# Kernel optimization log

Hardware: AMD Instinct MI355X
Metric: run time of the kernel (lower is better)

The kernel has to match this reference:

```python
import jax, jax.numpy as jnp
import numpy as np

H, T, D = 16, 4096, 64
N_SEQ = 8  # packed sequences -> cu_seqlens has N_SEQ+1 entries


def setup_inputs() -> dict:
    key = jax.random.key(0)
    kq, kk, kv, kc = jax.random.split(key, 4)
    q = jax.random.normal(kq, (1, H, T, D), dtype=jnp.float32)
    k = jax.random.normal(kk, (1, H, T, D), dtype=jnp.float32)
    v = jax.random.normal(kv, (1, H, T, D), dtype=jnp.float32)
    # cu_seqlens: monotonically increasing offsets, starts at 0, ends at T
    interior = jnp.sort(jax.random.randint(kc, (N_SEQ - 1,), 1, T, dtype=jnp.int32))
    cu_seqlens = jnp.concatenate([
        jnp.zeros((1,), jnp.int32), interior, jnp.full((1,), T, jnp.int32)
    ])
    return {"q": q, "k": k, "v": v, "cu_seqlens": cu_seqlens}


def reference(q, k, v, cu_seqlens):
    # Faithful to flash_attn_varlen_func(..., causal=False) on packed sequences:
    # non-causal attention restricted block-diagonally to each segment.
    scale = 1.0 / jnp.sqrt(jnp.asarray(D, q.dtype))
    # segment id for every token position
    pos = jnp.arange(T)
    seg = jnp.searchsorted(cu_seqlens[1:], pos, side="right")  # [T]
    mask = seg[:, None] == seg[None, :]                         # [T, T] block-diagonal
    # scores: [1, H, T, T]
    scores = jnp.einsum("bhqd,bhkd->bhqk", q, k) * scale
    neg = jnp.asarray(jnp.finfo(scores.dtype).min, scores.dtype)
    scores = jnp.where(mask[None, None], scores, neg)
    attn = jax.nn.softmax(scores, axis=-1)
    out = jnp.einsum("bhqk,bhkd->bhqd", attn, v)  # [1, H, T, D]
    return out
```

## Files before the change

kernel.cpp:

```cpp
#include <hip/hip_runtime.h>

#define HH 16
#define TT 4096
#define DD 64

typedef __attribute__((ext_vector_type(2))) __fp16 half2r;
typedef __attribute__((ext_vector_type(4))) _Float16 half4;
typedef __attribute__((ext_vector_type(4))) float float4v;

__global__ __launch_bounds__(256, 4) void pa_fwd(
    const float* __restrict__ qg, const float* __restrict__ kg,
    const float* __restrict__ vg, const int* __restrict__ cu,
    float* __restrict__ outg)
{
    __shared__ __align__(16) _Float16 Kl[2][64 * 64];
    __shared__ __align__(16) _Float16 Vl[2][64 * 64];

    const int tid  = threadIdx.x;
    const int lane = tid & 63;
    const int wave = tid >> 6;
    const int lr   = lane & 15;
    const int lg   = lane >> 4;

    const int bswz = ((int)blockIdx.x & 7) * 128 + ((int)blockIdx.x >> 3);
    const int h    = bswz >> 6;
    const int qblk = (bswz & 63) << 6;
    const int q    = qblk + wave * 16 + lr;

    int s = 0;
    while (cu[s + 1] <= q) ++s;
    const int lo = cu[s], hi = cu[s + 1];

    int sb = 0;
    while (cu[sb + 1] <= qblk) ++sb;
    const int blo = cu[sb];
    while (cu[sb + 1] <= qblk + 63) ++sb;
    const int bhi = cu[sb + 1];

    const int wlo = __shfl(lo, 0);
    const int whi = __shfl(hi, 15);
    const int mlo = __shfl(lo, 15);
    const int mhi = __shfl(hi, 0);

    const float qscale = 0.125f * 1.44269504088896f;
    const float* qrow = qg + ((size_t)h * TT + q) * DD;
    half4 qf[4];
#pragma unroll
    for (int ds = 0; ds < 4; ++ds) {
        float4v t4 = *(const float4v*)(qrow + ds * 16 + lg * 4);
        half2r a = __builtin_amdgcn_cvt_pkrtz(t4[0] * qscale, t4[1] * qscale);
        half2r b = __builtin_amdgcn_cvt_pkrtz(t4[2] * qscale, t4[3] * qscale);
        qf[ds][0] = (_Float16)a[0]; qf[ds][1] = (_Float16)a[1];
        qf[ds][2] = (_Float16)b[0]; qf[ds][3] = (_Float16)b[1];
    }

    const float* kh_ = kg + (size_t)h * TT * DD;
    const float* vh_ = vg + (size_t)h * TT * DD;

    const int srow = tid >> 2;
    const int sch  = (tid & 3) << 4;
    const int vd   = tid & 63;

    unsigned kwr[4], vwr[4];
#pragma unroll
    for (int i = 0; i < 4; ++i) {
        const int ko8 = (tid & 3) * 4 + i;
        kwr[i] = (unsigned)(srow * 128 + 16 * ((ko8 >> 1) ^ (srow & 7)) +
                            8 * ((ko8 & 1) ^ ((srow >> 3) & 1)));
        const int vo8 = wave * 4 + i;
        vwr[i] = (unsigned)(vd * 128 + 16 * ((vo8 >> 1) ^ (vd & 7)) +
                            8 * ((vo8 & 1) ^ ((vd >> 3) & 1)));
    }
    unsigned rbase[4];
#pragma unroll
    for (int i = 0; i < 4; ++i)
        rbase[i] = (unsigned)(lr * 128 + 16 * (((2 * i + (lg >> 1))) ^ (lr & 7)) +
                              8 * ((lg & 1) ^ ((lr >> 3) & 1)));

    float4v kq[4];
    float vv[16];

#define ISSUE(KT)                                                              \
    {                                                                          \
        const float4v* kp = (const float4v*)(kh_ + (size_t)((KT) + srow) * DD + sch); \
        kq[0] = kp[0]; kq[1] = kp[1]; kq[2] = kp[2]; kq[3] = kp[3];            \
        const float* vp = vh_ + (size_t)((KT) + wave * 16) * DD + vd;          \
        _Pragma("unroll")                                                      \
        for (int c = 0; c < 16; ++c) vv[c] = vp[c * DD];                       \
    }

    const int t0k = blo & ~63;
    ISSUE(t0k);

    float4v acc[4];
#pragma unroll
    for (int dt = 0; dt < 4; ++dt) acc[dt] = (float4v){0.f, 0.f, 0.f, 0.f};
    float m_run = -1e30f, lsum = 0.f;

    int cur = 0;
    for (int kt = t0k; kt < bhi; kt += 64) {
        {
            char* Kb = (char*)Kl[cur];
            char* Vb = (char*)Vl[cur];
#pragma unroll
            for (int i = 0; i < 4; ++i) {
                half2r a = __builtin_amdgcn_cvt_pkrtz(kq[i][0], kq[i][1]);
                half2r b = __builtin_amdgcn_cvt_pkrtz(kq[i][2], kq[i][3]);
                half4 hk;
                hk[0] = (_Float16)a[0]; hk[1] = (_Float16)a[1];
                hk[2] = (_Float16)b[0]; hk[3] = (_Float16)b[1];
                *(half4*)(Kb + kwr[i]) = hk;
            }
#pragma unroll
            for (int i = 0; i < 4; ++i) {
                half2r a = __builtin_amdgcn_cvt_pkrtz(vv[4 * i], vv[4 * i + 1]);
                half2r b = __builtin_amdgcn_cvt_pkrtz(vv[4 * i + 2], vv[4 * i + 3]);
                half4 hv;
                hv[0] = (_Float16)a[0]; hv[1] = (_Float16)a[1];
                hv[2] = (_Float16)b[0]; hv[3] = (_Float16)b[1];
                *(half4*)(Vb + vwr[i]) = hv;
            }
        }
        __syncthreads();

        if (kt + 64 < bhi) ISSUE(kt + 64);

        if (!(kt + 64 <= wlo || kt >= whi)) {
            const char* Kb = (const char*)Kl[cur];
            const char* Vb = (const char*)Vl[cur];

            float st[4][4];
            const bool fullv = (kt >= mlo) && (kt + 64 <= mhi);
            __builtin_amdgcn_s_setprio(1);
#pragma unroll
            for (int t = 0; t < 4; ++t) {
                float4v sa = (float4v){0.f, 0.f, 0.f, 0.f};
#pragma unroll
                for (int ds = 0; ds < 4; ++ds) {
                    half4 kf = *(const half4*)(Kb + rbase[ds] + t * 2048);
                    sa = __builtin_amdgcn_mfma_f32_16x16x16f16(kf, qf[ds], sa, 0, 0, 0);
                }
                if (fullv) {
#pragma unroll
                    for (int j = 0; j < 4; ++j) st[t][j] = sa[j];
                } else {
#pragma unroll
                    for (int j = 0; j < 4; ++j) {
                        const int key = kt + t * 16 + lg * 4 + j;
                        st[t][j] = (key >= lo && key < hi) ? sa[j] : -1e30f;
                    }
                }
            }
            __builtin_amdgcn_s_setprio(0);

            float tx = -1e30f;
#pragma unroll
            for (int t = 0; t < 4; ++t)
#pragma unroll
                for (int j = 0; j < 4; ++j) tx = fmaxf(tx, st[t][j]);
            tx = fmaxf(tx, __shfl_xor(tx, 16));
            tx = fmaxf(tx, __shfl_xor(tx, 32));

            if (__any(tx > m_run + 11.54f)) {
                const float mn = fmaxf(m_run, tx);
                const float a  = exp2f(m_run - mn);
                lsum *= a;
#pragma unroll
                for (int dt = 0; dt < 4; ++dt)
#pragma unroll
                    for (int j = 0; j < 4; ++j) acc[dt][j] *= a;
                m_run = mn;
            }

            half4 pb[4];
            float ps = 0.f;
#pragma unroll
            for (int t = 0; t < 4; ++t) {
                float e0 = exp2f(st[t][0] - m_run);
                float e1 = exp2f(st[t][1] - m_run);
                float e2 = exp2f(st[t][2] - m_run);
                float e3 = exp2f(st[t][3] - m_run);
                ps += (e0 + e1) + (e2 + e3);
                half2r a = __builtin_amdgcn_cvt_pkrtz(e0, e1);
                half2r b = __builtin_amdgcn_cvt_pkrtz(e2, e3);
                pb[t][0] = (_Float16)a[0]; pb[t][1] = (_Float16)a[1];
                pb[t][2] = (_Float16)b[0]; pb[t][3] = (_Float16)b[1];
            }
            ps += __shfl_xor(ps, 16);
            ps += __shfl_xor(ps, 32);
            lsum += ps;

            __builtin_amdgcn_s_setprio(1);
#pragma unroll
            for (int t = 0; t < 4; ++t)
#pragma unroll
                for (int dt = 0; dt < 4; ++dt) {
                    half4 vf = *(const half4*)(Vb + rbase[t] + dt * 2048);
                    acc[dt] = __builtin_amdgcn_mfma_f32_16x16x16f16(vf, pb[t], acc[dt], 0, 0, 0);
                }
            __builtin_amdgcn_s_setprio(0);
        }
        cur ^= 1;
    }

    const float inv = 1.0f / lsum;
    float* orow = outg + ((size_t)h * TT + q) * DD;
#pragma unroll
    for (int dt = 0; dt < 4; ++dt) {
        float4v o;
#pragma unroll
        for (int j = 0; j < 4; ++j) o[j] = acc[dt][j] * inv;
        *(float4v*)(orow + dt * 16 + lg * 4) = o;
    }
#undef ISSUE
}

extern "C" void kernel_launch(void* const* d_in, const int* in_sizes, int n_in,
                              void* d_out, int out_size, void* d_ws, size_t ws_size,
                              hipStream_t stream) {
    const float* q  = (const float*)d_in[0];
    const float* k  = (const float*)d_in[1];
    const float* v  = (const float*)d_in[2];
    const int*   cu = (const int*)d_in[3];
    float* out = (float*)d_out;

    dim3 grid(HH * (TT / 64));
    dim3 block(256);
    hipLaunchKernelGGL(pa_fwd, grid, block, 0, stream, q, k, v, cu, out);
}
```

Baseline: 90.51 us.

## Use 16x16x32 MFMA for QK^T and vectorize K/V LDS staging

Replaces the four 16x16x16 f16 MFMAs per score tile with two 16x16x32 MFMAs, loading K fragments as 8-wide halves from LDS and Q as half8. It also restructures the global-to-LDS staging: K/V are written as 16-byte half8 stores with a new XOR swizzle, V is loaded as float2 pairs, and pointers are advanced incrementally instead of being recomputed. The goal is to cut MFMA issue count, LDS instruction count and address arithmetic. The price is a new swizzle layout that must stay consistent between the write and read paths.

```diff
diff --git a/kernel.cpp b/kernel.cpp
--- a/kernel.cpp
+++ b/kernel.cpp
@@ -6,6 +6,8 @@
 
 typedef __attribute__((ext_vector_type(2))) __fp16 half2r;
 typedef __attribute__((ext_vector_type(4))) _Float16 half4;
+typedef __attribute__((ext_vector_type(8))) _Float16 half8;
+typedef __attribute__((ext_vector_type(2))) float float2v;
 typedef __attribute__((ext_vector_type(4))) float float4v;
 
 __global__ __launch_bounds__(256, 4) void pa_fwd(
@@ -44,53 +46,59 @@
 
     const float qscale = 0.125f * 1.44269504088896f;
     const float* qrow = qg + ((size_t)h * TT + q) * DD;
-    half4 qf[4];
-#pragma unroll
-    for (int ds = 0; ds < 4; ++ds) {
-        float4v t4 = *(const float4v*)(qrow + ds * 16 + lg * 4);
-        half2r a = __builtin_amdgcn_cvt_pkrtz(t4[0] * qscale, t4[1] * qscale);
-        half2r b = __builtin_amdgcn_cvt_pkrtz(t4[2] * qscale, t4[3] * qscale);
-        qf[ds][0] = (_Float16)a[0]; qf[ds][1] = (_Float16)a[1];
-        qf[ds][2] = (_Float16)b[0]; qf[ds][3] = (_Float16)b[1];
+    half8 qf8[2];
+#pragma unroll
+    for (int ds = 0; ds < 2; ++ds) {
+        const float* qp = qrow + ds * 32 + lg * 8;
+        float4v a = *(const float4v*)qp;
+        float4v b = *(const float4v*)(qp + 4);
+        half2r p0 = __builtin_amdgcn_cvt_pkrtz(a[0] * qscale, a[1] * qscale);
+        half2r p1 = __builtin_amdgcn_cvt_pkrtz(a[2] * qscale, a[3] * qscale);
+        half2r p2 = __builtin_amdgcn_cvt_pkrtz(b[0] * qscale, b[1] * qscale);
+        half2r p3 = __builtin_amdgcn_cvt_pkrtz(b[2] * qscale, b[3] * qscale);
+        qf8[ds][0] = (_Float16)p0[0]; qf8[ds][1] = (_Float16)p0[1];
+        qf8[ds][2] = (_Float16)p1[0]; qf8[ds][3] = (_Float16)p1[1];
+        qf8[ds][4] = (_Float16)p2[0]; qf8[ds][5] = (_Float16)p2[1];
+        qf8[ds][6] = (_Float16)p3[0]; qf8[ds][7] = (_Float16)p3[1];
     }
 
     const float* kh_ = kg + (size_t)h * TT * DD;
     const float* vh_ = vg + (size_t)h * TT * DD;
 
     const int srow = tid >> 2;
-    const int sch  = (tid & 3) << 4;
-    const int vd   = tid & 63;
-
-    unsigned kwr[4], vwr[4];
-#pragma unroll
-    for (int i = 0; i < 4; ++i) {
-        const int ko8 = (tid & 3) * 4 + i;
-        kwr[i] = (unsigned)(srow * 128 + 16 * ((ko8 >> 1) ^ (srow & 7)) +
-                            8 * ((ko8 & 1) ^ ((srow >> 3) & 1)));
-        const int vo8 = wave * 4 + i;
-        vwr[i] = (unsigned)(vd * 128 + 16 * ((vo8 >> 1) ^ (vd & 7)) +
-                            8 * ((vo8 & 1) ^ ((vd >> 3) & 1)));
-    }
-    unsigned rbase[4];
-#pragma unroll
-    for (int i = 0; i < 4; ++i)
-        rbase[i] = (unsigned)(lr * 128 + 16 * (((2 * i + (lg >> 1))) ^ (lr & 7)) +
-                              8 * ((lg & 1) ^ ((lr >> 3) & 1)));
+    const int sc   = tid & 3;
+    const unsigned kwrA = (unsigned)(srow * 128 + (((2 * sc)     ^ (srow & 7)) << 4));
+    const unsigned kwrB = (unsigned)(srow * 128 + (((2 * sc + 1) ^ (srow & 7)) << 4));
+    const int vd2 = tid & 31;
+    const int vko = tid >> 5;
+    const int vr0 = 2 * vd2, vr1 = 2 * vd2 + 1;
+    const unsigned vwrA = (unsigned)(vr0 * 128 + ((vko ^ (vr0 & 7)) << 4));
+    const unsigned vwrB = (unsigned)(vr1 * 128 + ((vko ^ (vr1 & 7)) << 4));
+
+    const unsigned kb0 = (unsigned)(lr * 128 + (((lg)     ^ (lr & 7)) << 4));
+    const unsigned kb1 = (unsigned)(lr * 128 + (((4 + lg) ^ (lr & 7)) << 4));
+    unsigned vrb[4];
+#pragma unroll
+    for (int t = 0; t < 4; ++t)
+        vrb[t] = (unsigned)(lr * 128 + (((2 * t + (lg >> 1)) ^ (lr & 7)) << 4) +
+                            ((lg & 1) << 3));
 
     float4v kq[4];
-    float vv[16];
-
-#define ISSUE(KT)                                                              \
+    float2v vv2[8];
+    const int t0k = blo & ~63;
+    const float4v* kp = (const float4v*)(kh_ + (size_t)(t0k + srow) * DD + sc * 16);
+    const float*   vp = vh_ + (size_t)(t0k + vko * 8) * DD + vd2 * 2;
+
+#define ISSUE()                                                                \
     {                                                                          \
-        const float4v* kp = (const float4v*)(kh_ + (size_t)((KT) + srow) * DD + sch); \
         kq[0] = kp[0]; kq[1] = kp[1]; kq[2] = kp[2]; kq[3] = kp[3];            \
-        const float* vp = vh_ + (size_t)((KT) + wave * 16) * DD + vd;          \
+        kp += (64 * DD) / 4;                                                   \
         _Pragma("unroll")                                                      \
-        for (int c = 0; c < 16; ++c) vv[c] = vp[c * DD];                       \
-    }
-
-    const int t0k = blo & ~63;
-    ISSUE(t0k);
+        for (int c = 0; c < 8; ++c) vv2[c] = *(const float2v*)(vp + c * DD);   \
+        vp += 64 * DD;                                                         \
+    }
+
+    ISSUE();
 
     float4v acc[4];
 #pragma unroll
@@ -102,28 +110,33 @@
         {
             char* Kb = (char*)Kl[cur];
             char* Vb = (char*)Vl[cur];
-#pragma unroll
-            for (int i = 0; i < 4; ++i) {
+            half8 hk0, hk1, hv0, hv1;
+#pragma unroll
+            for (int i = 0; i < 2; ++i) {
                 half2r a = __builtin_amdgcn_cvt_pkrtz(kq[i][0], kq[i][1]);
                 half2r b = __builtin_amdgcn_cvt_pkrtz(kq[i][2], kq[i][3]);
-                half4 hk;
-                hk[0] = (_Float16)a[0]; hk[1] = (_Float16)a[1];
-                hk[2] = (_Float16)b[0]; hk[3] = (_Float16)b[1];
-                *(half4*)(Kb + kwr[i]) = hk;
+                hk0[4 * i + 0] = (_Float16)a[0]; hk0[4 * i + 1] = (_Float16)a[1];
+                hk0[4 * i + 2] = (_Float16)b[0]; hk0[4 * i + 3] = (_Float16)b[1];
+                half2r c2 = __builtin_amdgcn_cvt_pkrtz(kq[2 + i][0], kq[2 + i][1]);
+                half2r d2 = __builtin_amdgcn_cvt_pkrtz(kq[2 + i][2], kq[2 + i][3]);
+                hk1[4 * i + 0] = (_Float16)c2[0]; hk1[4 * i + 1] = (_Float16)c2[1];
+                hk1[4 * i + 2] = (_Float16)d2[0]; hk1[4 * i + 3] = (_Float16)d2[1];
             }
 #pragma unroll
             for (int i = 0; i < 4; ++i) {
-                half2r a = __builtin_amdgcn_cvt_pkrtz(vv[4 * i], vv[4 * i + 1]);
-                half2r b = __builtin_amdgcn_cvt_pkrtz(vv[4 * i + 2], vv[4 * i + 3]);
-                half4 hv;
-                hv[0] = (_Float16)a[0]; hv[1] = (_Float16)a[1];
-                hv[2] = (_Float16)b[0]; hv[3] = (_Float16)b[1];
-                *(half4*)(Vb + vwr[i]) = hv;
-            }
+                half2r a = __builtin_amdgcn_cvt_pkrtz(vv2[2 * i][0], vv2[2 * i + 1][0]);
+                half2r b = __builtin_amdgcn_cvt_pkrtz(vv2[2 * i][1], vv2[2 * i + 1][1]);
+                hv0[2 * i] = (_Float16)a[0]; hv0[2 * i + 1] = (_Float16)a[1];
+                hv1[2 * i] = (_Float16)b[0]; hv1[2 * i + 1] = (_Float16)b[1];
+            }
+            *(half8*)(Kb + kwrA) = hk0;
+            *(half8*)(Kb + kwrB) = hk1;
+            *(half8*)(Vb + vwrA) = hv0;
+            *(half8*)(Vb + vwrB) = hv1;
         }
         __syncthreads();
 
-        if (kt + 64 < bhi) ISSUE(kt + 64);
+        if (kt + 64 < bhi) ISSUE();
 
         if (!(kt + 64 <= wlo || kt >= whi)) {
             const char* Kb = (const char*)Kl[cur];
@@ -135,11 +148,10 @@
 #pragma unroll
             for (int t = 0; t < 4; ++t) {
                 float4v sa = (float4v){0.f, 0.f, 0.f, 0.f};
-#pragma unroll
-                for (int ds = 0; ds < 4; ++ds) {
-                    half4 kf = *(const half4*)(Kb + rbase[ds] + t * 2048);
-                    sa = __builtin_amdgcn_mfma_f32_16x16x16f16(kf, qf[ds], sa, 0, 0, 0);
-                }
+                half8 kf0 = *(const half8*)(Kb + kb0 + t * 2048);
+                half8 kf1 = *(const half8*)(Kb + kb1 + t * 2048);
+                sa = __builtin_amdgcn_mfma_f32_16x16x32_f16(kf0, qf8[0], sa, 0, 0, 0);
+                sa = __builtin_amdgcn_mfma_f32_16x16x32_f16(kf1, qf8[1], sa, 0, 0, 0);
                 if (fullv) {
 #pragma unroll
                     for (int j = 0; j < 4; ++j) st[t][j] = sa[j];
@@ -153,11 +165,14 @@
             }
             __builtin_amdgcn_s_setprio(0);
 
-            float tx = -1e30f;
-#pragma unroll
-            for (int t = 0; t < 4; ++t)
-#pragma unroll
-                for (int j = 0; j < 4; ++j) tx = fmaxf(tx, st[t][j]);
+            float tx = fmaxf(fmaxf(st[0][0], st[0][1]), st[0][2]);
+            tx = fmaxf(fmaxf(tx, st[0][3]), st[1][0]);
+            tx = fmaxf(fmaxf(tx, st[1][1]), st[1][2]);
+            tx = fmaxf(fmaxf(tx, st[1][3]), st[2][0]);
+            tx = fmaxf(fmaxf(tx, st[2][1]), st[2][2]);
+            tx = fmaxf(fmaxf(tx, st[2][3]), st[3][0]);
+            tx = fmaxf(fmaxf(tx, st[3][1]), st[3][2]);
+            tx = fmaxf(tx, st[3][3]);
             tx = fmaxf(tx, __shfl_xor(tx, 16));
             tx = fmaxf(tx, __shfl_xor(tx, 32));
 
@@ -195,7 +210,7 @@
             for (int t = 0; t < 4; ++t)
 #pragma unroll
                 for (int dt = 0; dt < 4; ++dt) {
-                    half4 vf = *(const half4*)(Vb + rbase[t] + dt * 2048);
+                    half4 vf = *(const half4*)(Vb + vrb[t] + dt * 2048);
                     acc[dt] = __builtin_amdgcn_mfma_f32_16x16x16f16(vf, pb[t], acc[dt], 0, 0, 0);
                 }
             __builtin_amdgcn_s_setprio(0);
```

Result: no change. 89.44 us (-1.2%).
